# Performance work log

Measured on AMD Instinct MI355X. Metric: run time of the kernel, lower is better.

The kernel has to match this reference:

```python
import jax, jax.numpy as jnp
import numpy as np
from jax import lax

B, T, H, K = 64, 512, 768, 13


def setup_inputs() -> dict:
    key = jax.random.key(0)
    ks = jax.random.split(key, 6)
    hidden_states = jax.random.normal(ks[0], (B, T, H), dtype=jnp.float32)
    labels = jax.random.randint(ks[1], (B, T), 0, K, dtype=jnp.int64)
    attention_mask = jnp.ones((B, T), dtype=jnp.int32)  # torchcrf requires mask[:,0]=1
    W = jax.random.normal(ks[2], (H, K), dtype=jnp.float32) * 0.02
    b = jnp.zeros((K,), dtype=jnp.float32)
    start_transitions = jax.random.uniform(ks[3], (K,), minval=-0.1, maxval=0.1)
    end_transitions = jax.random.uniform(ks[4], (K,), minval=-0.1, maxval=0.1)
    transitions = jax.random.uniform(ks[5], (K, K), minval=-0.1, maxval=0.1)
    return {"hidden_states": hidden_states, "labels": labels,
            "attention_mask": attention_mask, "W": W, "b": b,
            "start_transitions": start_transitions,
            "end_transitions": end_transitions, "transitions": transitions}


def _crf_llh(emissions, tags, mask, start, end, trans):
    # emissions [B,T,K], tags [B,T] int, mask [B,T] bool
    Bn = emissions.shape[0]
    bidx = jnp.arange(Bn)
    maskf = mask.astype(emissions.dtype)

    # ---- numerator: score of the given tag sequence (vectorized gathers) ----
    tag_em = jnp.take_along_axis(emissions, tags[..., None], axis=2)[..., 0]  # [B,T]
    trans_sc = trans[tags[:, :-1], tags[:, 1:]]                               # [B,T-1]
    numerator = (start[tags[:, 0]] + tag_em[:, 0]
                 + jnp.sum((trans_sc + tag_em[:, 1:]) * maskf[:, 1:], axis=1))
    seq_ends = jnp.sum(mask.astype(jnp.int32), axis=1) - 1
    numerator = numerator + end[tags[bidx, seq_ends]]

    # ---- denominator: log partition via forward algorithm (scan over T) ----
    alpha0 = start[None, :] + emissions[:, 0]  # [B,K]

    def step(alpha, xs):
        em_t, m_t = xs  # [B,K], [B]
        nxt = jax.nn.logsumexp(alpha[:, :, None] + trans[None] + em_t[:, None, :], axis=1)
        alpha = jnp.where(m_t[:, None], nxt, alpha)
        return alpha, None

    xs = (jnp.swapaxes(emissions[:, 1:], 0, 1), jnp.swapaxes(mask[:, 1:], 0, 1))
    alpha, _ = lax.scan(step, alpha0, xs)
    denominator = jax.nn.logsumexp(alpha + end[None, :], axis=1)

    return jnp.sum(numerator - denominator)  # torchcrf default reduction='sum'


def reference(hidden_states, labels, attention_mask, W, b,
              start_transitions, end_transitions, transitions):
    # dropout is identity in eval mode
    logits = jnp.einsum('bth,hk->btk', hidden_states, W) + b  # [B,T,K]
    mask = attention_mask.astype(bool)
    llh = _crf_llh(logits, labels, mask, start_transitions,
                   end_transitions, transitions)
    loss = -1.0 * llh
    return (loss, logits)
```

## Files before the change

### kernel.cpp

```cpp
#include <hip/hip_runtime.h>
#include <hip/hip_bf16.h>

#define LOG2E 1.4426950408889634f
#define LN2   0.69314718055994531f

__device__ __forceinline__ float lse13(const float (&x)[13]) {
  float m = fmaxf(fmaxf(fmaxf(fmaxf(x[0], x[1]), fmaxf(x[2], x[3])),
                        fmaxf(fmaxf(x[4], x[5]), fmaxf(x[6], x[7]))),
                  fmaxf(fmaxf(fmaxf(x[8], x[9]), fmaxf(x[10], x[11])), x[12]));
  float s = (((exp2f(x[0] - m) + exp2f(x[1] - m)) + (exp2f(x[2] - m) + exp2f(x[3] - m))) +
             ((exp2f(x[4] - m) + exp2f(x[5] - m)) + (exp2f(x[6] - m) + exp2f(x[7] - m)))) +
            (((exp2f(x[8] - m) + exp2f(x[9] - m)) + (exp2f(x[10] - m) + exp2f(x[11] - m))) +
             exp2f(x[12] - m));
  return m + log2f(s);
}

__global__ __launch_bounds__(256) void k1_logits(const float* __restrict__ hs,
                                                 const float* __restrict__ W,
                                                 const float* __restrict__ bias,
                                                 float* __restrict__ logits) {
  __shared__ float wt[13 * 776];
  for (int idx = threadIdx.x; idx < 13 * 768; idx += 256) {
    int h = idx / 13;
    int k = idx - h * 13;
    wt[k * 776 + h] = W[idx];
  }
  __syncthreads();
  const int lane = threadIdx.x & 63;
  const int wid = (blockIdx.x << 2) + (threadIdx.x >> 6);
  const int nw = gridDim.x << 2;
  const int rr = lane / 13;
  const int kk = lane - rr * 13;
  const float bmine = (lane < 52) ? bias[kk] : 0.0f;

  for (int g = wid; g < 8192; g += nw) {
    const int r0 = g << 2;
    const float* hp = hs + (size_t)r0 * 768 + (lane << 2);
    float4 h[4][3];
#pragma unroll
    for (int r = 0; r < 4; ++r)
#pragma unroll
      for (int q = 0; q < 3; ++q)
        h[r][q] = *(const float4*)(hp + r * 768 + q * 256);
    float acc[4][13];
#pragma unroll
    for (int r = 0; r < 4; ++r)
#pragma unroll
      for (int k = 0; k < 13; ++k) acc[r][k] = 0.0f;
#pragma unroll
    for (int q = 0; q < 3; ++q) {
#pragma unroll
      for (int k = 0; k < 13; ++k) {
        const float4 w = *(const float4*)&wt[k * 776 + q * 256 + (lane << 2)];
#pragma unroll
        for (int r = 0; r < 4; ++r)
          acc[r][k] += h[r][q].x * w.x + h[r][q].y * w.y + h[r][q].z * w.z + h[r][q].w * w.w;
      }
    }
#pragma unroll
    for (int off = 32; off; off >>= 1)
#pragma unroll
      for (int r = 0; r < 4; ++r)
#pragma unroll
        for (int k = 0; k < 13; ++k)
          acc[r][k] += __shfl_xor(acc[r][k], off);
    if (lane < 52) {
      float v = acc[0][0];
#pragma unroll
      for (int r = 0; r < 4; ++r)
#pragma unroll
        for (int k = 0; k < 13; ++k)
          if (lane == r * 13 + k) v = acc[r][k];
      logits[(size_t)r0 * 13 + lane] = v + bmine;
    }
  }
}

__global__ __launch_bounds__(64) void k2a_chunks(const float* __restrict__ logits,
                                                 const int* __restrict__ amask,
                                                 const float* __restrict__ trans,
                                                 float* __restrict__ wsQ) {
  const int bc = blockIdx.x;
  const int b = bc >> 5;
  const int c = bc & 31;
  const int t0 = 1 + (c << 4);
  const int nt = min(16, 512 - t0);
  const int tid = threadIdx.x;
  __shared__ float trs[13 * 14];
  __shared__ float ems[16 * 14];
  __shared__ int msk[16];
  __shared__ float P[2][13 * 20];

  for (int idx = tid; idx < 169; idx += 64) {
    int i = idx / 13;
    int jj = idx - i * 13;
    trs[i * 14 + jj] = trans[idx] * LOG2E;
  }
  for (int idx = tid; idx < nt * 13; idx += 64) {
    int ts = idx / 13;
    int jj = idx - ts * 13;
    ems[ts * 14 + jj] = logits[((size_t)(b << 9) + t0 + ts) * 13 + jj] * LOG2E;
  }
  if (tid < nt) msk[tid] = amask[(b << 9) + t0 + tid];
  __syncthreads();

  int cr[3], cj[3];
  bool cv[3];
#pragma unroll
  for (int s = 0; s < 3; ++s) {
    const int cell = tid + (s << 6);
    cv[s] = cell < 169;
    const int cc = cv[s] ? cell : 0;
    cr[s] = cc / 13;
    cj[s] = cc - cr[s] * 13;
  }
  float tr[3][13];
#pragma unroll
  for (int s = 0; s < 3; ++s)
#pragma unroll
    for (int i = 0; i < 13; ++i) tr[s][i] = trs[i * 14 + cj[s]];

  int cur = 0;
  bool inited = false;
  for (int ts = 0; ts < nt; ++ts) {
    if (msk[ts]) {
      if (!inited) {
#pragma unroll
        for (int s = 0; s < 3; ++s)
          if (cv[s]) P[cur][cr[s] * 20 + cj[s]] = trs[cr[s] * 14 + cj[s]] + ems[ts * 14 + cj[s]];
        inited = true;
      } else {
#pragma unroll
        for (int s = 0; s < 3; ++s) {
          if (cv[s]) {
            const float* pr = &P[cur][cr[s] * 20];
            float x[13];
#pragma unroll
            for (int i = 0; i < 13; ++i) x[i] = pr[i] + tr[s][i];
            P[cur ^ 1][cr[s] * 20 + cj[s]] = lse13(x) + ems[ts * 14 + cj[s]];
          }
        }
        cur ^= 1;
      }
    }
  }
#pragma unroll
  for (int s = 0; s < 3; ++s) {
    if (cv[s]) {
      float v;
      if (inited) v = P[cur][cr[s] * 20 + cj[s]];
      else v = (cr[s] == cj[s]) ? 0.0f : -1e30f;
      wsQ[(size_t)bc * 169 + tid + (s << 6)] = v;
    }
  }
}

__global__ __launch_bounds__(64) void k2b_combine(const float* __restrict__ logits,
                                                  const int* __restrict__ labels,
                                                  const int* __restrict__ amask,
                                                  const float* __restrict__ stt,
                                                  const float* __restrict__ endt,
                                                  const float* __restrict__ trans,
                                                  const float* __restrict__ wsQ,
                                                  float* __restrict__ outb) {
  const int b = blockIdx.x;
  const int lane = threadIdx.x;
  float contrib = 0.0f;
  int msum = 0;
#pragma unroll
  for (int it = 0; it < 8; ++it) {
    const int t = (it << 6) + lane;
    const int base = (b << 9) + t;
    const int tag = labels[base];
    const int mk = amask[base];
    msum += mk;
    const float em = logits[(size_t)base * 13 + tag];
    if (t == 0) contrib += stt[tag] + em;
    else if (mk) contrib += trans[labels[base - 1] * 13 + tag] + em;
  }
#pragma unroll
  for (int off = 32; off; off >>= 1) {
    contrib += __shfl_xor(contrib, off);
    msum += __shfl_xor(msum, off);
  }
  const float num = contrib + endt[labels[(b << 9) + msum - 1]];
  const int j = (lane < 13) ? lane : 0;
  float a = (stt[j] + logits[(size_t)(b << 9) * 13 + j]) * LOG2E;
  const float* Qb = wsQ + (size_t)b * (32 * 169);
  float q[13];
#pragma unroll
  for (int i = 0; i < 13; ++i) q[i] = Qb[i * 13 + j];
  for (int c = 0; c < 32; ++c) {
    float qn[13];
    if (c + 1 < 32) {
      const float* Qn = Qb + (c + 1) * 169;
#pragma unroll
      for (int i = 0; i < 13; ++i) qn[i] = Qn[i * 13 + j];
    }
    float x[13];
#pragma unroll
    for (int i = 0; i < 13; ++i) {
      const float ai = __int_as_float(__builtin_amdgcn_readlane(__float_as_int(a), i));
      x[i] = ai + q[i];
    }
    a = lse13(x);
#pragma unroll
    for (int i = 0; i < 13; ++i) q[i] = qn[i];
  }
  float z = (lane < 13) ? (a + endt[lane] * LOG2E) : -1e30f;
  float mz = z;
#pragma unroll
  for (int off = 32; off; off >>= 1) mz = fmaxf(mz, __shfl_xor(mz, off));
  float ez = exp2f(z - mz);
#pragma unroll
  for (int off = 32; off; off >>= 1) ez += __shfl_xor(ez, off);
  if (lane == 0) outb[b] = num - (mz + log2f(ez)) * LN2;
}

__global__ __launch_bounds__(64) void k3_final(const float* __restrict__ outb,
                                               float* __restrict__ out) {
  float v = outb[threadIdx.x];
#pragma unroll
  for (int off = 32; off; off >>= 1) v += __shfl_xor(v, off);
  if (threadIdx.x == 0) out[0] = -v;
}

extern "C" void kernel_launch(void* const* d_in, const int* in_sizes, int n_in,
                              void* d_out, int out_size, void* d_ws, size_t ws_size,
                              hipStream_t stream) {
  const float* hs = (const float*)d_in[0];
  const int* labels = (const int*)d_in[1];
  const int* amask = (const int*)d_in[2];
  const float* W = (const float*)d_in[3];
  const float* bias = (const float*)d_in[4];
  const float* stt = (const float*)d_in[5];
  const float* endt = (const float*)d_in[6];
  const float* trans = (const float*)d_in[7];

  float* out = (float*)d_out;
  float* logits = out + 1;
  float* wsQ = (float*)d_ws;
  float* outb = wsQ + 64 * 32 * 169 + 64;

  k1_logits<<<1024, 256, 0, stream>>>(hs, W, bias, logits);
  k2a_chunks<<<64 * 32, 64, 0, stream>>>(logits, amask, trans, wsQ);
  k2b_combine<<<64, 64, 0, stream>>>(logits, labels, amask, stt, endt, trans, wsQ, outb);
  k3_final<<<1, 64, 0, stream>>>(outb, out);
}
```

Measured before the change: 258.1 us.

## Compute logits GEMM with split-bf16 MFMA and fold final reduction into atomics

Replaces the scalar FP32 logits projection with a matrix-core kernel. It splits both activations and weights into bf16 hi/lo parts and issues three 16x16x32 bf16 MFMAs per step to keep near-FP32 accuracy. A tiny pre-kernel packs W into that MFMA fragment layout and zeroes the output scalar. The separate final reduction kernel is removed: each batch block atomically adds its negated log-likelihood, which makes the float summation order nondeterministic.

```diff
diff --git a/kernel.cpp b/kernel.cpp
--- a/kernel.cpp
+++ b/kernel.cpp
@@ -3,6 +3,16 @@
 
 #define LOG2E 1.4426950408889634f
 #define LN2   0.69314718055994531f
+
+typedef __attribute__((ext_vector_type(8))) short short8;
+typedef __attribute__((ext_vector_type(4))) float f32x4;
+
+__device__ __forceinline__ unsigned bfbits(__bf16 x) {
+  return (unsigned)__builtin_bit_cast(unsigned short, x);
+}
+__device__ __forceinline__ unsigned cvt2bf(float a, float b) {
+  return bfbits((__bf16)a) | (bfbits((__bf16)b) << 16);
+}
 
 __device__ __forceinline__ float lse13(const float (&x)[13]) {
   float m = fmaxf(fmaxf(fmaxf(fmaxf(x[0], x[1]), fmaxf(x[2], x[3])),
@@ -15,64 +25,74 @@
   return m + log2f(s);
 }
 
-__global__ __launch_bounds__(256) void k1_logits(const float* __restrict__ hs,
-                                                 const float* __restrict__ W,
-                                                 const float* __restrict__ bias,
-                                                 float* __restrict__ logits) {
-  __shared__ float wt[13 * 776];
-  for (int idx = threadIdx.x; idx < 13 * 768; idx += 256) {
-    int h = idx / 13;
-    int k = idx - h * 13;
-    wt[k * 776 + h] = W[idx];
-  }
-  __syncthreads();
-  const int lane = threadIdx.x & 63;
-  const int wid = (blockIdx.x << 2) + (threadIdx.x >> 6);
-  const int nw = gridDim.x << 2;
-  const int rr = lane / 13;
-  const int kk = lane - rr * 13;
-  const float bmine = (lane < 52) ? bias[kk] : 0.0f;
-
-  for (int g = wid; g < 8192; g += nw) {
-    const int r0 = g << 2;
-    const float* hp = hs + (size_t)r0 * 768 + (lane << 2);
-    float4 h[4][3];
+__global__ __launch_bounds__(64) void k0_packW(const float* __restrict__ W,
+                                               uint4* __restrict__ pwsHi,
+                                               uint4* __restrict__ pwsLo,
+                                               float* __restrict__ out0) {
+  const int lane = threadIdx.x;
+  const int g = lane >> 4;
+  const int n = lane & 15;
+  for (int kk = 0; kk < 24; ++kk) {
+    unsigned hw[4], lw[4];
+#pragma unroll
+    for (int p = 0; p < 4; ++p) {
+      const int h0 = kk * 32 + g * 8 + 2 * p;
+      float v0 = (n < 13) ? W[h0 * 13 + n] : 0.0f;
+      float v1 = (n < 13) ? W[(h0 + 1) * 13 + n] : 0.0f;
+      __bf16 b0 = (__bf16)v0, b1 = (__bf16)v1;
+      float r0 = v0 - (float)b0, r1 = v1 - (float)b1;
+      hw[p] = bfbits(b0) | (bfbits(b1) << 16);
+      lw[p] = cvt2bf(r0, r1);
+    }
+    pwsHi[kk * 64 + lane] = make_uint4(hw[0], hw[1], hw[2], hw[3]);
+    pwsLo[kk * 64 + lane] = make_uint4(lw[0], lw[1], lw[2], lw[3]);
+  }
+  if (lane == 0) out0[0] = 0.0f;
+}
+
+__global__ __launch_bounds__(64) void k1_logits_mfma(const float* __restrict__ hs,
+                                                     const uint4* __restrict__ pwsHi,
+                                                     const uint4* __restrict__ pwsLo,
+                                                     const float* __restrict__ bias,
+                                                     float* __restrict__ logits) {
+  const int lane = threadIdx.x;
+  const int g = lane >> 4;
+  const int n = lane & 15;
+
+  const size_t row = (size_t)blockIdx.x * 16 + n;
+  const float* ap = hs + row * 768 + g * 8;
+  f32x4 acc = {0.0f, 0.0f, 0.0f, 0.0f};
+
+#pragma unroll 6
+  for (int kk = 0; kk < 24; ++kk) {
+    const float4 a0 = *(const float4*)(ap + kk * 32);
+    const float4 a1 = *(const float4*)(ap + kk * 32 + 4);
+    const uint4 wh = pwsHi[kk * 64 + lane];
+    const uint4 wl = pwsLo[kk * 64 + lane];
+    float v[8] = {a0.x, a0.y, a0.z, a0.w, a1.x, a1.y, a1.z, a1.w};
+    unsigned hw[4], lw[4];
+#pragma unroll
+    for (int p = 0; p < 4; ++p) {
+      float x0 = v[2 * p], x1 = v[2 * p + 1];
+      __bf16 b0 = (__bf16)x0, b1 = (__bf16)x1;
+      float r0 = x0 - (float)b0, r1 = x1 - (float)b1;
+      hw[p] = bfbits(b0) | (bfbits(b1) << 16);
+      lw[p] = cvt2bf(r0, r1);
+    }
+    const short8 ahi = __builtin_bit_cast(short8, make_uint4(hw[0], hw[1], hw[2], hw[3]));
+    const short8 alo = __builtin_bit_cast(short8, make_uint4(lw[0], lw[1], lw[2], lw[3]));
+    const short8 bhi = __builtin_bit_cast(short8, wh);
+    const short8 blo = __builtin_bit_cast(short8, wl);
+    acc = __builtin_amdgcn_mfma_f32_16x16x32_bf16(ahi, bhi, acc, 0, 0, 0);
+    acc = __builtin_amdgcn_mfma_f32_16x16x32_bf16(alo, bhi, acc, 0, 0, 0);
+    acc = __builtin_amdgcn_mfma_f32_16x16x32_bf16(ahi, blo, acc, 0, 0, 0);
+  }
+
+  if (n < 13) {
+    const float bj = bias[n];
 #pragma unroll
     for (int r = 0; r < 4; ++r)
-#pragma unroll
-      for (int q = 0; q < 3; ++q)
-        h[r][q] = *(const float4*)(hp + r * 768 + q * 256);
-    float acc[4][13];
-#pragma unroll
-    for (int r = 0; r < 4; ++r)
-#pragma unroll
-      for (int k = 0; k < 13; ++k) acc[r][k] = 0.0f;
-#pragma unroll
-    for (int q = 0; q < 3; ++q) {
-#pragma unroll
-      for (int k = 0; k < 13; ++k) {
-        const float4 w = *(const float4*)&wt[k * 776 + q * 256 + (lane << 2)];
-#pragma unroll
-        for (int r = 0; r < 4; ++r)
-          acc[r][k] += h[r][q].x * w.x + h[r][q].y * w.y + h[r][q].z * w.z + h[r][q].w * w.w;
-      }
-    }
-#pragma unroll
-    for (int off = 32; off; off >>= 1)
-#pragma unroll
-      for (int r = 0; r < 4; ++r)
-#pragma unroll
-        for (int k = 0; k < 13; ++k)
-          acc[r][k] += __shfl_xor(acc[r][k], off);
-    if (lane < 52) {
-      float v = acc[0][0];
-#pragma unroll
-      for (int r = 0; r < 4; ++r)
-#pragma unroll
-        for (int k = 0; k < 13; ++k)
-          if (lane == r * 13 + k) v = acc[r][k];
-      logits[(size_t)r0 * 13 + lane] = v + bmine;
-    }
+      logits[((size_t)blockIdx.x * 16 + g * 4 + r) * 13 + n] = acc[r] + bj;
   }
 }
 
@@ -162,7 +182,7 @@
                                                   const float* __restrict__ endt,
                                                   const float* __restrict__ trans,
                                                   const float* __restrict__ wsQ,
-                                                  float* __restrict__ outb) {
+                                                  float* __restrict__ out0) {
   const int b = blockIdx.x;
   const int lane = threadIdx.x;
   float contrib = 0.0f;
@@ -214,15 +234,10 @@
   float ez = exp2f(z - mz);
 #pragma unroll
   for (int off = 32; off; off >>= 1) ez += __shfl_xor(ez, off);
-  if (lane == 0) outb[b] = num - (mz + log2f(ez)) * LN2;
-}
-
-__global__ __launch_bounds__(64) void k3_final(const float* __restrict__ outb,
-                                               float* __restrict__ out) {
-  float v = outb[threadIdx.x];
-#pragma unroll
-  for (int off = 32; off; off >>= 1) v += __shfl_xor(v, off);
-  if (threadIdx.x == 0) out[0] = -v;
+  if (lane == 0) {
+    const float llh = num - (mz + log2f(ez)) * LN2;
+    atomicAdd(out0, -llh);
+  }
 }
 
 extern "C" void kernel_launch(void* const* d_in, const int* in_sizes, int n_in,
@@ -239,11 +254,13 @@
 
   float* out = (float*)d_out;
   float* logits = out + 1;
-  float* wsQ = (float*)d_ws;
-  float* outb = wsQ + 64 * 32 * 169 + 64;
-
-  k1_logits<<<1024, 256, 0, stream>>>(hs, W, bias, logits);
+
+  uint4* pwsHi = (uint4*)d_ws;
+  uint4* pwsLo = pwsHi + 24 * 64;
+  float* wsQ = (float*)(pwsLo + 24 * 64);
+
+  k0_packW<<<1, 64, 0, stream>>>(W, pwsHi, pwsLo, out);
+  k1_logits_mfma<<<2048, 64, 0, stream>>>(hs, pwsHi, pwsLo, bias, logits);
   k2a_chunks<<<64 * 32, 64, 0, stream>>>(logits, amask, trans, wsQ);
-  k2b_combine<<<64, 64, 0, stream>>>(logits, labels, amask, stt, endt, trans, wsQ, outb);
-  k3_final<<<1, 64, 0, stream>>>(outb, out);
-}
+  k2b_combine<<<64, 64, 0, stream>>>(logits, labels, amask, stt, endt, trans, wsQ, out);
+}
```

Result: faster. 229.1 us (-11.2%).
